# Optimization experiments

Hardware: AMD Instinct MI355X
Metric: run time of the kernel (lower is better)

Reference implementation:

```python
import jax, jax.numpy as jnp
import numpy as np

N = 100_000   # nodes
E = 1_600_000 # edges (avg degree 16)
IN_DIM = 128
OUT_DIM = 64
NEG_SLOPE = 0.2  # PyG GATConv default


def setup_inputs() -> dict:
    key = jax.random.key(0)
    k_x, k_ei, k_w, k_as, k_ad = jax.random.split(key, 5)
    x = jax.random.normal(k_x, (N, IN_DIM), dtype=jnp.float32)
    edge_index = jax.random.randint(k_ei, (2, E), 0, N, dtype=jnp.int32)
    # GATConv params (heads=1): linear weight, attention vectors, output bias
    W = jax.random.normal(k_w, (IN_DIM, OUT_DIM), dtype=jnp.float32) / np.sqrt(IN_DIM)
    a_src = jax.random.normal(k_as, (OUT_DIM,), dtype=jnp.float32) * 0.1
    a_dst = jax.random.normal(k_ad, (OUT_DIM,), dtype=jnp.float32) * 0.1
    bias = jnp.zeros((OUT_DIM,), dtype=jnp.float32)
    return {"x": x, "edge_index": edge_index, "W": W, "a_src": a_src, "a_dst": a_dst, "bias": bias}


def reference(x, edge_index, W, a_src, a_dst, bias):
    # PyG GATConv, heads=1, add_self_loops=True
    h = x @ W                                   # [N, OUT]
    loop = jnp.arange(N, dtype=edge_index.dtype)
    ei = jnp.concatenate([edge_index, jnp.stack([loop, loop])], axis=1)  # [2, E+N]
    src, dst = ei[0], ei[1]
    # per-node attention logits, gathered per edge
    alpha_s = h @ a_src                         # [N]
    alpha_d = h @ a_dst                         # [N]
    e = alpha_s[src] + alpha_d[dst]             # [E+N]
    e = jnp.where(e > 0, e, NEG_SLOPE * e)      # leaky_relu
    # segment softmax over edges sharing the same destination node
    m = jax.ops.segment_max(e, dst, num_segments=N)   # every node has a self loop
    ex = jnp.exp(e - m[dst])
    s = jax.ops.segment_sum(ex, dst, num_segments=N)
    alpha = ex / s[dst]                         # [E+N]
    # weighted scatter-add of source messages
    out = jax.ops.segment_sum(alpha[:, None] * h[src], dst, num_segments=N)  # [N, OUT]
    return out + bias
```

## Files before the change

### kernel.cpp

```cpp
#include <hip/hip_runtime.h>
#include <hip/hip_bf16.h>

#ifndef NEG_SLOPE
#define NEG_SLOPE 0.2f
#endif

#define GRP_SHIFT 9
#define GRP_SIZE 512
#define NGMAX 256
#define MS_CHUNK 4096
#define BKT_CAP 10240

typedef short bf16x8 __attribute__((ext_vector_type(8)));
typedef float f32x4 __attribute__((ext_vector_type(4)));

__device__ __forceinline__ unsigned short f2bf(float f) {
    union { float f; unsigned int u; } c; c.f = f;
    unsigned int r = (c.u + 0x7FFFu + ((c.u >> 16) & 1u)) >> 16;
    return (unsigned short)r;
}
__device__ __forceinline__ float bf2f(unsigned short u) {
    union { unsigned int u; float f; } c; c.u = ((unsigned int)u) << 16;
    return c.f;
}
__device__ __forceinline__ float bflo(unsigned int u) {
    union { unsigned int u; float f; } c; c.u = u << 16;
    return c.f;
}
__device__ __forceinline__ float bfhi(unsigned int u) {
    union { unsigned int u; float f; } c; c.u = u & 0xffff0000u;
    return c.f;
}

struct GemmSmem {
    unsigned short xb[64 * 136];
    unsigned short wt[64 * 136];
};
struct MsSmem {
    unsigned int pack[MS_CHUNK];
    unsigned char gtag[MS_CHUNK];
    int hist[NGMAX];
    int gb[NGMAX];
    int wsum[4];
};
union FusedSmem {
    GemmSmem g;
    MsSmem m;
};

__global__ __launch_bounds__(256) void gemm_ms_kernel(
    const float* __restrict__ x, const float* __restrict__ W,
    const float* __restrict__ a_src, const float* __restrict__ a_dst,
    unsigned short* __restrict__ hb, float* __restrict__ as_,
    float* __restrict__ ad_, const int* __restrict__ ei,
    int* __restrict__ cursor, unsigned int* __restrict__ pairs,
    int N, int E, int NG, int nchunk)
{
    __shared__ FusedSmem sm;
    const int tid = threadIdx.x;

    if ((int)blockIdx.x < nchunk) {
        unsigned int* ls_pack = sm.m.pack;
        unsigned char* ls_g = sm.m.gtag;
        int* ls_hist = sm.m.hist;
        int* ls_gb = sm.m.gb;
        int* ls_wsum = sm.m.wsum;

        const int cs = (int)blockIdx.x * MS_CHUNK;
        const int n = min(MS_CHUNK, E - cs);
        const int* srcp = ei + cs;
        const int* dstp = ei + E + cs;

        ls_hist[tid] = 0;
        __syncthreads();
        for (int i = tid; i < n; i += 256)
            atomicAdd(&ls_hist[dstp[i] >> GRP_SHIFT], 1);
        __syncthreads();

        const int h = ls_hist[tid];
        const int lane = tid & 63;
        int incl = h;
#pragma unroll
        for (int off = 1; off < 64; off <<= 1) {
            const int t = __shfl_up(incl, off);
            if (lane >= off) incl += t;
        }
        const int wv = tid >> 6;
        if (lane == 63) ls_wsum[wv] = incl;
        __syncthreads();
        int wpre = 0;
        for (int w = 0; w < wv; ++w) wpre += ls_wsum[w];
        const int excl = wpre + incl - h;
        if (tid < NG && h > 0) {
            const int old = atomicAdd(&cursor[tid], h);
            ls_gb[tid] = tid * BKT_CAP + old - excl;
        }
        __syncthreads();
        ls_hist[tid] = excl;
        __syncthreads();

        for (int i = tid; i < n; i += 256) {
            const int src = srcp[i];
            const int dst = dstp[i];
            const int g = dst >> GRP_SHIFT;
            const int idx = atomicAdd(&ls_hist[g], 1);
            ls_pack[idx] = ((unsigned int)src << GRP_SHIFT) | (unsigned int)(dst & (GRP_SIZE - 1));
            ls_g[idx] = (unsigned char)g;
        }
        __syncthreads();

        for (int i = tid; i < n; i += 256) {
            const int g = ls_g[i];
            const int pos = ls_gb[g] + i;
            if (pos < (g + 1) * BKT_CAP)
                pairs[pos] = ls_pack[i];
        }
    } else {
        unsigned short* xb = sm.g.xb;
        unsigned short* wt = sm.g.wt;
        const int r0 = ((int)blockIdx.x - nchunk) * 64;

        for (int idx = tid; idx < 2048; idx += 256) {
            const int r = idx >> 5;
            const int c4 = idx & 31;
            const int row = r0 + r;
            float4 v = make_float4(0.f, 0.f, 0.f, 0.f);
            if (row < N) v = ((const float4*)(x + (size_t)row * 128))[c4];
            ushort4 o;
            o.x = f2bf(v.x); o.y = f2bf(v.y); o.z = f2bf(v.z); o.w = f2bf(v.w);
            *(ushort4*)(xb + r * 136 + c4 * 4) = o;
        }
        for (int idx = tid; idx < 4096; idx += 256) {
            const int k2 = idx >> 6;
            const int nn = idx & 63;
            const float a = W[(k2 * 2) * 64 + nn];
            const float b = W[(k2 * 2 + 1) * 64 + nn];
            ushort2 o;
            o.x = f2bf(a);
            o.y = f2bf(b);
            *(ushort2*)(wt + nn * 136 + k2 * 2) = o;
        }
        __syncthreads();

        const int wv = tid >> 6;
        const int lane = tid & 63;
        const int m16 = lane & 15;
        const int quad = lane >> 4;

        f32x4 acc[4];
#pragma unroll
        for (int ct = 0; ct < 4; ++ct) acc[ct] = (f32x4){0.f, 0.f, 0.f, 0.f};

        const unsigned short* xrow = xb + (wv * 16 + m16) * 136;
#pragma unroll
        for (int kq = 0; kq < 4; ++kq) {
            const int k0 = kq * 32;
            const bf16x8 a = *(const bf16x8*)(xrow + k0 + quad * 8);
#pragma unroll
            for (int ct = 0; ct < 4; ++ct) {
                const bf16x8 b = *(const bf16x8*)(wt + (ct * 16 + m16) * 136 + k0 + quad * 8);
                acc[ct] = __builtin_amdgcn_mfma_f32_16x16x32_bf16(a, b, acc[ct], 0, 0, 0);
            }
        }

#pragma unroll
        for (int ct = 0; ct < 4; ++ct) {
#pragma unroll
            for (int rg = 0; rg < 4; ++rg) {
                const int row = r0 + wv * 16 + quad * 4 + rg;
                if (row < N) hb[(size_t)row * 64 + ct * 16 + m16] = f2bf(acc[ct][rg]);
            }
        }

        float asv[4], adv[4];
#pragma unroll
        for (int ct = 0; ct < 4; ++ct) {
            asv[ct] = a_src[ct * 16 + m16];
            adv[ct] = a_dst[ct * 16 + m16];
        }
#pragma unroll
        for (int rg = 0; rg < 4; ++rg) {
            float ps = acc[0][rg] * asv[0] + acc[1][rg] * asv[1] +
                       acc[2][rg] * asv[2] + acc[3][rg] * asv[3];
            float pd = acc[0][rg] * adv[0] + acc[1][rg] * adv[1] +
                       acc[2][rg] * adv[2] + acc[3][rg] * adv[3];
#pragma unroll
            for (int off = 1; off < 16; off <<= 1) {
                ps += __shfl_xor(ps, off);
                pd += __shfl_xor(pd, off);
            }
            const int row = r0 + wv * 16 + quad * 4 + rg;
            if (m16 == 0 && row < N) { as_[row] = ps; ad_[row] = pd; }
        }
    }
}

__global__ __launch_bounds__(1024) void group_sort_kernel(
    const unsigned int* __restrict__ pairs, const int* __restrict__ cursor,
    unsigned int* __restrict__ meta, int* __restrict__ csr, int N)
{
    __shared__ int sdeg[GRP_SIZE];
    __shared__ int scur[GRP_SIZE];
    __shared__ int swsum[8];
    __shared__ int ssrc[BKT_CAP];
    const int g = blockIdx.x;
    const int tid = threadIdx.x;
    const int eb0 = g * BKT_CAP;
    const int cnt = min(cursor[g], BKT_CAP);

    if (tid < GRP_SIZE) sdeg[tid] = 0;
    __syncthreads();
    for (int i = tid; i < cnt; i += 1024)
        atomicAdd(&sdeg[pairs[eb0 + i] & (GRP_SIZE - 1)], 1);
    __syncthreads();

    int s = 0, incl = 0;
    if (tid < GRP_SIZE) {
        s = sdeg[tid];
        const int lane = tid & 63;
        incl = s;
#pragma unroll
        for (int off = 1; off < 64; off <<= 1) {
            const int t = __shfl_up(incl, off);
            if (lane >= off) incl += t;
        }
        if (lane == 63) swsum[tid >> 6] = incl;
    }
    __syncthreads();
    if (tid < GRP_SIZE) {
        int wpre = 0;
        const int wv = tid >> 6;
        for (int w = 0; w < wv; ++w) wpre += swsum[w];
        const int excl = wpre + incl - s;
        scur[tid] = excl;
        const int node = (g << GRP_SHIFT) + tid;
        if (node < N)
            meta[node] = ((unsigned int)(eb0 + excl) << 10) | (unsigned int)min(s, 1023);
    }
    __syncthreads();

    for (int i = tid; i < cnt; i += 1024) {
        const unsigned int p = pairs[eb0 + i];
        const int idx = atomicAdd(&scur[p & (GRP_SIZE - 1)], 1);
        ssrc[idx] = (int)(p >> GRP_SHIFT);
    }
    __syncthreads();
    for (int i = tid; i < cnt; i += 1024)
        csr[eb0 + i] = ssrc[i];
}

__device__ void aggregate_slow(
    const unsigned short* __restrict__ h, const float* __restrict__ as_,
    const float* __restrict__ ad_, const int* __restrict__ csr,
    const float* __restrict__ bias, float* __restrict__ out,
    int wid, int p0, int deg, int lane)
{
    const float adi = ad_[wid];
    float e0 = as_[wid] + adi;
    e0 = e0 > 0.f ? e0 : NEG_SLOPE * e0;
    float m = e0, ll = 1.f;
    float acc = bf2f(h[(size_t)wid * 64 + lane]);
    const int p1 = p0 + deg;
    for (int p = p0; p < p1; ++p) {
        const int sj = csr[p];
        float ee = as_[sj] + adi;
        ee = ee > 0.f ? ee : NEG_SLOPE * ee;
        const float nm = fmaxf(m, ee);
        const float sc = __expf(m - nm);
        const float pp = __expf(ee - nm);
        ll = ll * sc + pp;
        acc = acc * sc + pp * bf2f(h[(size_t)sj * 64 + lane]);
        m = nm;
    }
    out[(size_t)wid * 64 + lane] = acc / ll + bias[lane];
}

__global__ __launch_bounds__(256) void aggregate_kernel(
    const unsigned short* __restrict__ h, const float* __restrict__ as_,
    const float* __restrict__ ad_, const unsigned int* __restrict__ meta,
    const int* __restrict__ csr, const float* __restrict__ bias,
    float* __restrict__ out, int N)
{
    const int wbase = (blockIdx.x * 256 + threadIdx.x) >> 6;
    const int lane = threadIdx.x & 63;
    const int widA = wbase * 2;
    if (widA >= N) return;
    const int widB = widA + 1;
    const bool hasB = (widB < N);

    const unsigned int mtA = meta[widA];
    const unsigned int mtB = hasB ? meta[widB] : 0u;
    const int p0A = (int)(mtA >> 10), degA = (int)(mtA & 1023u);
    const int p0B = (int)(mtB >> 10), degB = (int)(mtB & 1023u);

    if (degA <= 63 && degB <= 63) {
        const float adiA = ad_[widA];
        const float adiB = hasB ? ad_[widB] : 0.f;
        float e0A = as_[widA] + adiA;
        e0A = e0A > 0.f ? e0A : NEG_SLOPE * e0A;
        float e0B = hasB ? as_[widB] + adiB : 0.f;
        e0B = e0B > 0.f ? e0B : NEG_SLOPE * e0B;

        int sA = widA, sB = hasB ? widB : widA;
        float eA = -1e30f, eB = -1e30f;
        if (lane < degA) {
            sA = csr[p0A + lane];
            const float t = as_[sA] + adiA;
            eA = t > 0.f ? t : NEG_SLOPE * t;
        } else if (lane == degA) {
            eA = e0A;
        }
        if (hasB) {
            if (lane < degB) {
                sB = csr[p0B + lane];
                const float t = as_[sB] + adiB;
                eB = t > 0.f ? t : NEG_SLOPE * t;
            } else if (lane == degB) {
                eB = e0B;
            }
        }

        float mA = eA, mB = eB;
#pragma unroll
        for (int off = 1; off < 64; off <<= 1) {
            mA = fmaxf(mA, __shfl_xor(mA, off));
            mB = fmaxf(mB, __shfl_xor(mB, off));
        }
        const float peA = __expf(eA - mA);
        const float peB = hasB ? __expf(eB - mB) : 0.f;
        float lA = peA, lB = peB;
#pragma unroll
        for (int off = 1; off < 64; off <<= 1) {
            lA += __shfl_xor(lA, off);
            lB += __shfl_xor(lB, off);
        }

        const int half = lane >> 5;
        const int l5 = lane & 31;
        const unsigned int* hb32 = (const unsigned int*)h;
        float a0 = 0.f, a1 = 0.f, b0 = 0.f, b1 = 0.f;
        const int npA = (degA + 2) >> 1;
        const int npB = hasB ? (degB + 2) >> 1 : 0;
        const int npMax = max(npA, npB);

        for (int jp = 0; jp < npMax; jp += 4) {
            const int sl0 = (jp    ) * 2 + half;
            const int sl1 = (jp + 1) * 2 + half;
            const int sl2 = (jp + 2) * 2 + half;
            const int sl3 = (jp + 3) * 2 + half;
            const int sa0 = __shfl(sA, sl0), sa1 = __shfl(sA, sl1);
            const int sa2 = __shfl(sA, sl2), sa3 = __shfl(sA, sl3);
            const int sb0 = __shfl(sB, sl0), sb1 = __shfl(sB, sl1);
            const int sb2 = __shfl(sB, sl2), sb3 = __shfl(sB, sl3);
            const float wa0 = __shfl(peA, sl0), wa1 = __shfl(peA, sl1);
            const float wa2 = __shfl(peA, sl2), wa3 = __shfl(peA, sl3);
            const float wb0 = __shfl(peB, sl0), wb1 = __shfl(peB, sl1);
            const float wb2 = __shfl(peB, sl2), wb3 = __shfl(peB, sl3);
            const unsigned int ua0 = hb32[sa0 * 32 + l5];
            const unsigned int ua1 = hb32[sa1 * 32 + l5];
            const unsigned int ua2 = hb32[sa2 * 32 + l5];
            const unsigned int ua3 = hb32[sa3 * 32 + l5];
            const unsigned int ub0 = hb32[sb0 * 32 + l5];
            const unsigned int ub1 = hb32[sb1 * 32 + l5];
            const unsigned int ub2 = hb32[sb2 * 32 + l5];
            const unsigned int ub3 = hb32[sb3 * 32 + l5];
            a0 += wa0 * bflo(ua0); a1 += wa0 * bfhi(ua0);
            a0 += wa1 * bflo(ua1); a1 += wa1 * bfhi(ua1);
            a0 += wa2 * bflo(ua2); a1 += wa2 * bfhi(ua2);
            a0 += wa3 * bflo(ua3); a1 += wa3 * bfhi(ua3);
            b0 += wb0 * bflo(ub0); b1 += wb0 * bfhi(ub0);
            b0 += wb1 * bflo(ub1); b1 += wb1 * bfhi(ub1);
            b0 += wb2 * bflo(ub2); b1 += wb2 * bfhi(ub2);
            b0 += wb3 * bflo(ub3); b1 += wb3 * bfhi(ub3);
        }
        a0 += __shfl_xor(a0, 32);
        a1 += __shfl_xor(a1, 32);
        b0 += __shfl_xor(b0, 32);
        b1 += __shfl_xor(b1, 32);
        if (half == 0) {
            const float2 bv = ((const float2*)bias)[l5];
            float2 oA;
            oA.x = a0 / lA + bv.x;
            oA.y = a1 / lA + bv.y;
            ((float2*)(out + (size_t)widA * 64))[l5] = oA;
            if (hasB) {
                float2 oB;
                oB.x = b0 / lB + bv.x;
                oB.y = b1 / lB + bv.y;
                ((float2*)(out + (size_t)widB * 64))[l5] = oB;
            }
        }
    } else {
        aggregate_slow(h, as_, ad_, csr, bias, out, widA, p0A, degA, lane);
        if (hasB) aggregate_slow(h, as_, ad_, csr, bias, out, widB, p0B, degB, lane);
    }
}

extern "C" void kernel_launch(void* const* d_in, const int* in_sizes, int n_in,
                              void* d_out, int out_size, void* d_ws, size_t ws_size,
                              hipStream_t stream)
{
    const float* x     = (const float*)d_in[0];
    const int*   ei    = (const int*)d_in[1];
    const float* W     = (const float*)d_in[2];
    const float* a_src = (const float*)d_in[3];
    const float* a_dst = (const float*)d_in[4];
    const float* bias  = (const float*)d_in[5];
    float* out = (float*)d_out;

    const int N = in_sizes[0] / 128;
    const int E = in_sizes[1] / 2;
    const int NG = (N + GRP_SIZE - 1) >> GRP_SHIFT;
    const int nchunk = (E + MS_CHUNK - 1) / MS_CHUNK;
    const int gemmBlocks = (N + 63) / 64;

    unsigned short* hb = (unsigned short*)d_ws;
    float* alpha_s = (float*)(hb + (size_t)N * 64);
    float* alpha_d = alpha_s + N;
    int* cursor = (int*)(alpha_d + N);
    unsigned int* meta = (unsigned int*)(cursor + NG);
    int* csr = (int*)(meta + N);
    unsigned int* pairs = (unsigned int*)(csr + (size_t)NG * BKT_CAP);

    hipMemsetAsync(cursor, 0, (size_t)NG * sizeof(int), stream);
    gemm_ms_kernel<<<nchunk + gemmBlocks, 256, 0, stream>>>(
        x, W, a_src, a_dst, hb, alpha_s, alpha_d, ei, cursor, pairs,
        N, E, NG, nchunk);
    group_sort_kernel<<<NG, 1024, 0, stream>>>(pairs, cursor, meta, csr, N);
    aggregate_kernel<<<(N + 7) / 8, 256, 0, stream>>>(hb, alpha_s, alpha_d, meta,
                                                      csr, bias, out, N);
}
```

Before: 182.1 us.

## Replace two-level bucket sort with global degree count, scan, and atomic scatter CSR build

```diff
diff --git a/kernel.cpp b/kernel.cpp
--- a/kernel.cpp
+++ b/kernel.cpp
@@ -7,7 +7,6 @@
 
 #define GRP_SHIFT 9
 #define GRP_SIZE 512
-#define NGMAX 256
 #define MS_CHUNK 4096
 #define BKT_CAP 10240
 
@@ -35,17 +34,6 @@
 struct GemmSmem {
     unsigned short xb[64 * 136];
     unsigned short wt[64 * 136];
-};
-struct MsSmem {
-    unsigned int pack[MS_CHUNK];
-    unsigned char gtag[MS_CHUNK];
-    int hist[NGMAX];
-    int gb[NGMAX];
-    int wsum[4];
-};
-union FusedSmem {
-    GemmSmem g;
-    MsSmem m;
 };
 
 __global__ __launch_bounds__(256) void gemm_ms_kernel(
@@ -53,71 +41,21 @@
     const float* __restrict__ a_src, const float* __restrict__ a_dst,
     unsigned short* __restrict__ hb, float* __restrict__ as_,
     float* __restrict__ ad_, const int* __restrict__ ei,
-    int* __restrict__ cursor, unsigned int* __restrict__ pairs,
-    int N, int E, int NG, int nchunk)
-{
-    __shared__ FusedSmem sm;
+    int* __restrict__ deg,
+    int N, int E, int nchunk)
+{
+    __shared__ GemmSmem sm;
     const int tid = threadIdx.x;
 
     if ((int)blockIdx.x < nchunk) {
-        unsigned int* ls_pack = sm.m.pack;
-        unsigned char* ls_g = sm.m.gtag;
-        int* ls_hist = sm.m.hist;
-        int* ls_gb = sm.m.gb;
-        int* ls_wsum = sm.m.wsum;
-
         const int cs = (int)blockIdx.x * MS_CHUNK;
         const int n = min(MS_CHUNK, E - cs);
-        const int* srcp = ei + cs;
         const int* dstp = ei + E + cs;
-
-        ls_hist[tid] = 0;
-        __syncthreads();
         for (int i = tid; i < n; i += 256)
-            atomicAdd(&ls_hist[dstp[i] >> GRP_SHIFT], 1);
-        __syncthreads();
-
-        const int h = ls_hist[tid];
-        const int lane = tid & 63;
-        int incl = h;
-#pragma unroll
-        for (int off = 1; off < 64; off <<= 1) {
-            const int t = __shfl_up(incl, off);
-            if (lane >= off) incl += t;
-        }
-        const int wv = tid >> 6;
-        if (lane == 63) ls_wsum[wv] = incl;
-        __syncthreads();
-        int wpre = 0;
-        for (int w = 0; w < wv; ++w) wpre += ls_wsum[w];
-        const int excl = wpre + incl - h;
-        if (tid < NG && h > 0) {
-            const int old = atomicAdd(&cursor[tid], h);
-            ls_gb[tid] = tid * BKT_CAP + old - excl;
-        }
-        __syncthreads();
-        ls_hist[tid] = excl;
-        __syncthreads();
-
-        for (int i = tid; i < n; i += 256) {
-            const int src = srcp[i];
-            const int dst = dstp[i];
-            const int g = dst >> GRP_SHIFT;
-            const int idx = atomicAdd(&ls_hist[g], 1);
-            ls_pack[idx] = ((unsigned int)src << GRP_SHIFT) | (unsigned int)(dst & (GRP_SIZE - 1));
-            ls_g[idx] = (unsigned char)g;
-        }
-        __syncthreads();
-
-        for (int i = tid; i < n; i += 256) {
-            const int g = ls_g[i];
-            const int pos = ls_gb[g] + i;
-            if (pos < (g + 1) * BKT_CAP)
-                pairs[pos] = ls_pack[i];
-        }
+            atomicAdd(&deg[dstp[i]], 1);
     } else {
-        unsigned short* xb = sm.g.xb;
-        unsigned short* wt = sm.g.wt;
+        unsigned short* xb = sm.xb;
+        unsigned short* wt = sm.wt;
         const int r0 = ((int)blockIdx.x - nchunk) * 64;
 
         for (int idx = tid; idx < 2048; idx += 256) {
@@ -195,58 +133,48 @@
     }
 }
 
-__global__ __launch_bounds__(1024) void group_sort_kernel(
-    const unsigned int* __restrict__ pairs, const int* __restrict__ cursor,
-    unsigned int* __restrict__ meta, int* __restrict__ csr, int N)
-{
-    __shared__ int sdeg[GRP_SIZE];
-    __shared__ int scur[GRP_SIZE];
+__global__ __launch_bounds__(512) void scan_meta_kernel(
+    const int* __restrict__ deg, unsigned int* __restrict__ meta,
+    int* __restrict__ cur, int N)
+{
     __shared__ int swsum[8];
-    __shared__ int ssrc[BKT_CAP];
     const int g = blockIdx.x;
     const int tid = threadIdx.x;
+    const int node = (g << GRP_SHIFT) + tid;
     const int eb0 = g * BKT_CAP;
-    const int cnt = min(cursor[g], BKT_CAP);
-
-    if (tid < GRP_SIZE) sdeg[tid] = 0;
+
+    const int s = (node < N) ? deg[node] : 0;
+    const int lane = tid & 63;
+    int incl = s;
+#pragma unroll
+    for (int off = 1; off < 64; off <<= 1) {
+        const int t = __shfl_up(incl, off);
+        if (lane >= off) incl += t;
+    }
+    if (lane == 63) swsum[tid >> 6] = incl;
     __syncthreads();
-    for (int i = tid; i < cnt; i += 1024)
-        atomicAdd(&sdeg[pairs[eb0 + i] & (GRP_SIZE - 1)], 1);
-    __syncthreads();
-
-    int s = 0, incl = 0;
-    if (tid < GRP_SIZE) {
-        s = sdeg[tid];
-        const int lane = tid & 63;
-        incl = s;
-#pragma unroll
-        for (int off = 1; off < 64; off <<= 1) {
-            const int t = __shfl_up(incl, off);
-            if (lane >= off) incl += t;
-        }
-        if (lane == 63) swsum[tid >> 6] = incl;
-    }
-    __syncthreads();
-    if (tid < GRP_SIZE) {
-        int wpre = 0;
-        const int wv = tid >> 6;
-        for (int w = 0; w < wv; ++w) wpre += swsum[w];
-        const int excl = wpre + incl - s;
-        scur[tid] = excl;
-        const int node = (g << GRP_SHIFT) + tid;
-        if (node < N)
-            meta[node] = ((unsigned int)(eb0 + excl) << 10) | (unsigned int)min(s, 1023);
-    }
-    __syncthreads();
-
-    for (int i = tid; i < cnt; i += 1024) {
-        const unsigned int p = pairs[eb0 + i];
-        const int idx = atomicAdd(&scur[p & (GRP_SIZE - 1)], 1);
-        ssrc[idx] = (int)(p >> GRP_SHIFT);
-    }
-    __syncthreads();
-    for (int i = tid; i < cnt; i += 1024)
-        csr[eb0 + i] = ssrc[i];
+    int wpre = 0;
+    const int wv = tid >> 6;
+    for (int w = 0; w < wv; ++w) wpre += swsum[w];
+    const int excl = wpre + incl - s;
+    if (node < N) {
+        meta[node] = ((unsigned int)(eb0 + excl) << 10) | (unsigned int)min(s, 1023);
+        cur[node] = eb0 + excl;
+    }
+}
+
+__global__ __launch_bounds__(256) void scatter_kernel(
+    const int* __restrict__ ei, int* __restrict__ cur,
+    int* __restrict__ csr, int E)
+{
+    const int stride = gridDim.x * 256;
+    for (int i = (int)blockIdx.x * 256 + threadIdx.x; i < E; i += stride) {
+        const int src = ei[i];
+        const int dst = ei[E + i];
+        const int pos = atomicAdd(&cur[dst], 1);
+        if (pos < ((dst >> GRP_SHIFT) + 1) * BKT_CAP)
+            csr[pos] = src;
+    }
 }
 
 __device__ void aggregate_slow(
@@ -417,16 +345,16 @@
     unsigned short* hb = (unsigned short*)d_ws;
     float* alpha_s = (float*)(hb + (size_t)N * 64);
     float* alpha_d = alpha_s + N;
-    int* cursor = (int*)(alpha_d + N);
-    unsigned int* meta = (unsigned int*)(cursor + NG);
+    int* deg = (int*)(alpha_d + N);
+    int* cur = deg + N;
+    unsigned int* meta = (unsigned int*)(cur + N);
     int* csr = (int*)(meta + N);
-    unsigned int* pairs = (unsigned int*)(csr + (size_t)NG * BKT_CAP);
-
-    hipMemsetAsync(cursor, 0, (size_t)NG * sizeof(int), stream);
+
+    hipMemsetAsync(deg, 0, (size_t)N * sizeof(int), stream);
     gemm_ms_kernel<<<nchunk + gemmBlocks, 256, 0, stream>>>(
-        x, W, a_src, a_dst, hb, alpha_s, alpha_d, ei, cursor, pairs,
-        N, E, NG, nchunk);
-    group_sort_kernel<<<NG, 1024, 0, stream>>>(pairs, cursor, meta, csr, N);
+        x, W, a_src, a_dst, hb, alpha_s, alpha_d, ei, deg, N, E, nchunk);
+    scan_meta_kernel<<<NG, 512, 0, stream>>>(deg, meta, cur, N);
+    scatter_kernel<<<2048, 256, 0, stream>>>(ei, cur, csr, E);
     aggregate_kernel<<<(N + 7) / 8, 256, 0, stream>>>(hb, alpha_s, alpha_d, meta,
                                                       csr, bias, out, N);
 }
```

New measurement: 342.3 us. 1.88x slower.
